# Optimization experiments

Hardware: AMD Instinct MI355X
Metric: run time of the kernel (lower is better)

The kernel has to match this reference:

```python
import jax, jax.numpy as jnp
import numpy as np

B, H, W = 4, 256, 256
DIM = 180
NH = 6
WH, WW = 16, 16          # window size
BH, BW = 8, 8            # base window size
CH = DIM // (2 * NH)     # per-head dim = 15
SCALE = float(CH)        # note: divide by head_dim (not sqrt), as in source
RH, RW = WH // BH, WW // BW
R = RH * RW              # spatial reduction ratio = 4
L = WH * WW              # 256 tokens per window
BL = BH * BW             # 64 base tokens
POS_DIM = (DIM // 4) // 4  # 11


def _rel_index(Hs, Ws):
    coords = np.stack(np.meshgrid(np.arange(Hs), np.arange(Ws), indexing='ij')).reshape(2, -1)
    rel = (coords[:, :, None] - coords[:, None, :]).transpose(1, 2, 0)
    rel[..., 0] += Hs - 1
    rel[..., 1] += Ws - 1
    rel[..., 0] *= 2 * Ws - 1
    return rel.sum(-1)  # (L, L) int

RPI = _rel_index(WH, WW)


def _ln(x, g, b):
    mu = x.mean(-1, keepdims=True)
    var = ((x - mu) ** 2).mean(-1, keepdims=True)
    return (x - mu) / jnp.sqrt(var + 1e-5) * g + b


def _conv(x, w, b):  # x: NHWC, w: HWIO
    y = jax.lax.conv_general_dilated(x, w, (1, 1), 'SAME',
                                     dimension_numbers=('NHWC', 'HWIO', 'NHWC'))
    return y + b


def setup_inputs():
    key = jax.random.key(0)
    ks = jax.random.split(key, 12)
    def wgt(k, shape, s=0.05):
        return jax.random.normal(k, shape, jnp.float32) * s
    C5 = DIM // 5
    d = {}
    d['x'] = jax.random.normal(ks[0], (B, H, W, DIM), jnp.float32)
    d['dfe_c1_w'] = wgt(ks[1], (1, 1, DIM, C5)); d['dfe_c1_b'] = jnp.zeros((C5,), jnp.float32)
    d['dfe_c2_w'] = wgt(ks[2], (3, 3, C5, C5));  d['dfe_c2_b'] = jnp.zeros((C5,), jnp.float32)
    d['dfe_c3_w'] = wgt(ks[3], (1, 1, C5, DIM)); d['dfe_c3_b'] = jnp.zeros((DIM,), jnp.float32)
    d['dfe_lin_w'] = wgt(ks[4], (1, 1, DIM, DIM)); d['dfe_lin_b'] = jnp.zeros((DIM,), jnp.float32)
    d['sl_w'] = wgt(ks[5], (1, R), 0.5); d['sl_b'] = jnp.zeros((1,), jnp.float32)
    d['pos_proj_w'] = wgt(ks[6], (POS_DIM, 2), 0.1); d['pos_proj_b'] = jnp.zeros((POS_DIM,), jnp.float32)
    for i, kk in zip((1, 2), (ks[7], ks[8])):
        d['pos%d_ln_g' % i] = jnp.ones((POS_DIM,), jnp.float32)
        d['pos%d_ln_b' % i] = jnp.zeros((POS_DIM,), jnp.float32)
        d['pos%d_w' % i] = wgt(kk, (POS_DIM, POS_DIM), 0.1)
        d['pos%d_b' % i] = jnp.zeros((POS_DIM,), jnp.float32)
    d['pos3_ln_g'] = jnp.ones((POS_DIM,), jnp.float32)
    d['pos3_ln_b'] = jnp.zeros((POS_DIM,), jnp.float32)
    d['pos3_w'] = wgt(ks[9], (NH, POS_DIM), 0.1)
    d['pos3_b'] = jnp.zeros((NH,), jnp.float32)
    d['proj_w'] = wgt(ks[10], (DIM, DIM))
    d['proj_b'] = jnp.zeros((DIM,), jnp.float32)
    return d


def reference(x, dfe_c1_w, dfe_c1_b, dfe_c2_w, dfe_c2_b, dfe_c3_w, dfe_c3_b,
              dfe_lin_w, dfe_lin_b, sl_w, sl_b, pos_proj_w, pos_proj_b,
              pos1_ln_g, pos1_ln_b, pos1_w, pos1_b,
              pos2_ln_g, pos2_ln_b, pos2_w, pos2_b,
              pos3_ln_g, pos3_ln_b, pos3_w, pos3_b,
              proj_w, proj_b):
    Bb, Hh, Ww_, C = x.shape
    # ---- DFE: qv = conv_path(x) * linear_path(x) ----
    t = jax.nn.leaky_relu(_conv(x, dfe_c1_w, dfe_c1_b), 0.2)
    t = jax.nn.leaky_relu(_conv(t, dfe_c2_w, dfe_c2_b), 0.2)
    t = _conv(t, dfe_c3_w, dfe_c3_b)
    qv = t * _conv(x, dfe_lin_w, dfe_lin_b)  # (B,H,W,C)
    # ---- window partition ----
    qv = qv.reshape(Bb, Hh // WH, WH, Ww_ // WW, WW, C).transpose(0, 1, 3, 2, 4, 5)
    qv = qv.reshape(-1, L, C)                       # (B_, L, C)
    B_ = qv.shape[0]
    qv = qv.reshape(B_, L, 2, NH, CH)
    q = qv[:, :, 0].transpose(0, 2, 1, 3)           # (B_, NH, L, CH)
    v = qv[:, :, 1].transpose(0, 2, 1, 3)           # (B_, NH, L, CH)
    # ---- spatial linear projection of v to base window ----
    vp = v.reshape(B_, NH, BH, RH, BW, RW, CH).transpose(0, 1, 2, 4, 6, 3, 5)
    vp = vp.reshape(B_, NH, BL, CH, R)
    vp = jnp.einsum('bnlcr,r->bnlc', vp, sl_w[0]) + sl_b[0]  # (B_, NH, BL, CH)
    # ---- spatial self-correlation ----
    corr = jnp.einsum('bnlc,bnmc->bnlm', q, vp) / SCALE       # (B_, NH, L, BL)
    # dynamic relative position bias (non-residual MLP)
    ph = jnp.arange(1 - WH, WH)
    pw = jnp.arange(1 - WW, WW)
    biases = jnp.stack(jnp.meshgrid(ph, pw, indexing='ij')).reshape(2, -1).T.astype(x.dtype)
    p = biases @ pos_proj_w.T + pos_proj_b
    p = jax.nn.relu(_ln(p, pos1_ln_g, pos1_ln_b)) @ pos1_w.T + pos1_b
    p = jax.nn.relu(_ln(p, pos2_ln_g, pos2_ln_b)) @ pos2_w.T + pos2_b
    pos = jax.nn.relu(_ln(p, pos3_ln_g, pos3_ln_b)) @ pos3_w.T + pos3_b  # ((2WH-1)(2WW-1), NH)
    rpb = pos[RPI.reshape(-1)].reshape(L, L, NH).transpose(2, 0, 1)      # (NH, L, L)
    rpb = rpb.reshape(NH, L, BH, RH, BW, RW).transpose(0, 1, 2, 4, 3, 5)
    rpb = rpb.reshape(NH, L, BL, R).mean(-1)                             # (NH, L, BL)
    corr = corr + rpb[None]
    x_sp = jnp.einsum('bnlm,bnmc->bnlc', corr, vp)
    x_sp = x_sp.transpose(0, 2, 1, 3).reshape(B_, L, C // 2)
    # ---- channel self-correlation (single-head) ----
    qc = q.transpose(0, 2, 1, 3).reshape(B_, L, C // 2)
    vc = v.transpose(0, 2, 1, 3).reshape(B_, L, C // 2)
    cmap = jnp.einsum('blc,bld->bcd', qc, vc) / float(L)                 # (B_, C/2, C/2)
    x_ch = jnp.einsum('bcd,bld->blc', cmap, vc)                          # (B_, L, C/2)
    # ---- window reverse + fuse ----
    def rev(a):
        c = a.shape[-1]
        a = a.reshape(Bb, Hh // WH, Ww_ // WW, WH, WW, c).transpose(0, 1, 3, 2, 4, 5)
        return a.reshape(Bb, Hh, Ww_, c)
    x_sp = rev(x_sp.reshape(B_, WH, WW, C // 2))
    x_ch = rev(x_ch.reshape(B_, WH, WW, C // 2))
    out = jnp.concatenate([x_sp, x_ch], -1) @ proj_w.T + proj_b          # (B,H,W,C)
    return out
```

## Files before the change

kernel.cpp:

```cpp
#include <hip/hip_runtime.h>

#define LEAKY(v) ((v) > 0.f ? (v) : 0.2f * (v))

__device__ __forceinline__ void ln_relu11(float* p, const float* __restrict__ g,
                                          const float* __restrict__ b) {
  float mu = 0.f;
#pragma unroll
  for (int j = 0; j < 11; ++j) mu += p[j];
  mu *= (1.f / 11.f);
  float var = 0.f;
#pragma unroll
  for (int j = 0; j < 11; ++j) { float d = p[j] - mu; var += d * d; }
  var *= (1.f / 11.f);
  float inv = 1.f / sqrtf(var + 1e-5f);
#pragma unroll
  for (int j = 0; j < 11; ++j) {
    float v = (p[j] - mu) * inv * g[j] + b[j];
    p[j] = v > 0.f ? v : 0.f;
  }
}

__global__ void pos_mlp_kernel(
    const float* __restrict__ w0, const float* __restrict__ b0,
    const float* __restrict__ g1, const float* __restrict__ be1,
    const float* __restrict__ w1, const float* __restrict__ b1,
    const float* __restrict__ g2, const float* __restrict__ be2,
    const float* __restrict__ w2, const float* __restrict__ b2,
    const float* __restrict__ g3, const float* __restrict__ be3,
    const float* __restrict__ w3, const float* __restrict__ b3,
    float* __restrict__ pos_out) {
  int r = blockIdx.x * 256 + threadIdx.x;
  if (r >= 961) return;
  float bh = (float)(r / 31 - 15);
  float bw = (float)(r % 31 - 15);
  float p[11], q[11];
#pragma unroll
  for (int j = 0; j < 11; ++j) p[j] = bh * w0[2 * j] + bw * w0[2 * j + 1] + b0[j];
  ln_relu11(p, g1, be1);
#pragma unroll
  for (int j = 0; j < 11; ++j) {
    float s = b1[j];
#pragma unroll
    for (int k = 0; k < 11; ++k) s += p[k] * w1[j * 11 + k];
    q[j] = s;
  }
  ln_relu11(q, g2, be2);
#pragma unroll
  for (int j = 0; j < 11; ++j) {
    float s = b2[j];
#pragma unroll
    for (int k = 0; k < 11; ++k) s += q[k] * w2[j * 11 + k];
    p[j] = s;
  }
  ln_relu11(p, g3, be3);
#pragma unroll
  for (int n = 0; n < 6; ++n) {
    float s = b3[n];
#pragma unroll
    for (int k = 0; k < 11; ++k) s += p[k] * w3[n * 11 + k];
    pos_out[r * 6 + n] = s;
  }
}

__global__ void rpb_kernel(const float* __restrict__ pos, float* __restrict__ rpb) {
  int o = blockIdx.x * 256 + threadIdx.x;
  int n = o >> 14;
  int l = (o >> 6) & 255;
  int m = o & 63;
  int i1 = l >> 4, j1 = l & 15;
  int bi = m >> 3, bj = m & 7;
  float s = 0.f;
#pragma unroll
  for (int rh = 0; rh < 2; ++rh)
#pragma unroll
    for (int rw = 0; rw < 2; ++rw) {
      int i2 = bi * 2 + rh, j2 = bj * 2 + rw;
      int idx = (i1 - i2 + 15) * 31 + (j1 - j2 + 15);
      s += pos[idx * 6 + n];
    }
  rpb[o] = s * 0.25f;
}

__global__ void pt_kernel(const float* __restrict__ pjw, float* __restrict__ pt) {
  int i = blockIdx.x * 256 + threadIdx.x;
  if (i >= 180 * 180) return;
  int c = i / 180, k = i % 180;
  pt[c * 180 + k] = pjw[k * 180 + c];
}

__global__ __launch_bounds__(256) void dfe1_kernel(const float* __restrict__ x,
                                                   const float* __restrict__ w1,
                                                   const float* __restrict__ b1,
                                                   float* __restrict__ t1) {
  __shared__ float xt[256][36];
  int t = threadIdx.x;
  int p0 = blockIdx.x * 256;
  float acc[36];
#pragma unroll
  for (int j = 0; j < 36; ++j) acc[j] = 0.f;
  for (int kc = 0; kc < 5; ++kc) {
    __syncthreads();
    for (int idx = t; idx < 256 * 36; idx += 256) {
      int px = idx / 36, ci = idx % 36;
      xt[px][ci] = x[(p0 + px) * 180 + kc * 36 + ci];
    }
    __syncthreads();
    for (int ci = 0; ci < 36; ++ci) {
      float v = xt[t][ci];
      const float* wr = &w1[(kc * 36 + ci) * 36];
#pragma unroll
      for (int j = 0; j < 36; ++j) acc[j] += v * wr[j];
    }
  }
  float* o = &t1[(p0 + t) * 36];
#pragma unroll
  for (int j = 0; j < 36; ++j) {
    float v = acc[j] + b1[j];
    o[j] = LEAKY(v);
  }
}

__global__ __launch_bounds__(256) void dfe2_kernel(const float* __restrict__ t1,
                                                   const float* __restrict__ w2,
                                                   const float* __restrict__ b2,
                                                   float* __restrict__ t2) {
  __shared__ float halo[18][18][36];
  int t = threadIdx.x;
  int blk = blockIdx.x;
  int img = blk >> 8;
  int rem = blk & 255;
  int ty0 = (rem >> 4) << 4;
  int tx0 = (rem & 15) << 4;
  for (int idx = t; idx < 18 * 18 * 36; idx += 256) {
    int ci = idx % 36;
    int xx = (idx / 36) % 18;
    int yy = idx / (36 * 18);
    int gy = ty0 + yy - 1;
    int gx = tx0 + xx - 1;
    float v = 0.f;
    if (gy >= 0 && gy < 256 && gx >= 0 && gx < 256)
      v = t1[((img * 256 + gy) * 256 + gx) * 36 + ci];
    halo[yy][xx][ci] = v;
  }
  __syncthreads();
  int ly = t >> 4, lx = t & 15;
  float acc[36];
#pragma unroll
  for (int j = 0; j < 36; ++j) acc[j] = 0.f;
#pragma unroll
  for (int kh = 0; kh < 3; ++kh)
#pragma unroll
    for (int kw = 0; kw < 3; ++kw) {
      for (int ci = 0; ci < 36; ++ci) {
        float v = halo[ly + kh][lx + kw][ci];
        const float* wr = &w2[((kh * 3 + kw) * 36 + ci) * 36];
#pragma unroll
        for (int j = 0; j < 36; ++j) acc[j] += v * wr[j];
      }
    }
  float* o = &t2[((img * 256 + ty0 + ly) * 256 + tx0 + lx) * 36];
#pragma unroll
  for (int j = 0; j < 36; ++j) {
    float v = acc[j] + b2[j];
    o[j] = LEAKY(v);
  }
}

__global__ __launch_bounds__(256, 4) void dfe3_kernel(const float* __restrict__ x,
                                                      const float* __restrict__ t2,
                                                      const float* __restrict__ w3,
                                                      const float* __restrict__ b3,
                                                      const float* __restrict__ wl,
                                                      const float* __restrict__ bl,
                                                      float* __restrict__ qv) {
  __shared__ __align__(16) float As[36 * 68];
  __shared__ __align__(16) float Bs[36 * 180 + 16];
  int t = threadIdx.x;
  int tx = t & 15;
  int ty = t >> 4;
  int p0 = blockIdx.x * 64;

  int pa0 = t / 9,          ca0 = t - pa0 * 9;
  int pa1 = (t + 256) / 9,  ca1 = (t + 256) - pa1 * 9;
  int pa2 = (t + 512) / 9,  ca2 = (t + 512) - pa2 * 9;
  const float4* xf4  = (const float4*)x;
  const float4* t2f4 = (const float4*)t2;
  const float4* wlf4 = (const float4*)wl;
  const float4* w3f4 = (const float4*)w3;
  float4* Bs4 = (float4*)Bs;

  float4 aR0, aR1, aR2;
  float4 bR0, bR1, bR2, bR3, bR4, bR5, bR6;
  aR2 = make_float4(0.f, 0.f, 0.f, 0.f);
  bR6 = make_float4(0.f, 0.f, 0.f, 0.f);

  auto stage_write = [&]() {
    As[(ca0 * 4 + 0) * 68 + pa0] = aR0.x;
    As[(ca0 * 4 + 1) * 68 + pa0] = aR0.y;
    As[(ca0 * 4 + 2) * 68 + pa0] = aR0.z;
    As[(ca0 * 4 + 3) * 68 + pa0] = aR0.w;
    As[(ca1 * 4 + 0) * 68 + pa1] = aR1.x;
    As[(ca1 * 4 + 1) * 68 + pa1] = aR1.y;
    As[(ca1 * 4 + 2) * 68 + pa1] = aR1.z;
    As[(ca1 * 4 + 3) * 68 + pa1] = aR1.w;
    if (t < 64) {
      As[(ca2 * 4 + 0) * 68 + pa2] = aR2.x;
      As[(ca2 * 4 + 1) * 68 + pa2] = aR2.y;
      As[(ca2 * 4 + 2) * 68 + pa2] = aR2.z;
      As[(ca2 * 4 + 3) * 68 + pa2] = aR2.w;
    }
    Bs4[t] = bR0;
    Bs4[t + 256] = bR1;
    Bs4[t + 512] = bR2;
    Bs4[t + 768] = bR3;
    Bs4[t + 1024] = bR4;
    Bs4[t + 1280] = bR5;
    if (t < 84) Bs4[t + 1536] = bR6;
  };

  auto compute36 = [&](float acc[4][12]) {
    for (int ci = 0; ci < 36; ++ci) {
      float4 a = *(const float4*)&As[ci * 68 + ty * 4];
      const float* bp = &Bs[ci * 180 + tx * 12];
      float4 b0 = *(const float4*)bp;
      float4 b1 = *(const float4*)(bp + 4);
      float4 b2 = *(const float4*)(bp + 8);
      float av[4] = {a.x, a.y, a.z, a.w};
      float bv[12] = {b0.x, b0.y, b0.z, b0.w, b1.x, b1.y, b1.z, b1.w,
                      b2.x, b2.y, b2.z, b2.w};
#pragma unroll
      for (int r = 0; r < 4; ++r)
#pragma unroll
        for (int j = 0; j < 12; ++j) acc[r][j] += av[r] * bv[j];
    }
  };

  aR0 = xf4[(size_t)(p0 + pa0) * 45 + ca0];
  aR1 = xf4[(size_t)(p0 + pa1) * 45 + ca1];
  if (t < 64) aR2 = xf4[(size_t)(p0 + pa2) * 45 + ca2];
  bR0 = wlf4[t];
  bR1 = wlf4[t + 256];
  bR2 = wlf4[t + 512];
  bR3 = wlf4[t + 768];
  bR4 = wlf4[t + 1024];
  bR5 = wlf4[t + 1280];
  if (t < 84) bR6 = wlf4[t + 1536];

  float accL[4][12], accC[4][12];
#pragma unroll
  for (int r = 0; r < 4; ++r)
#pragma unroll
    for (int j = 0; j < 12; ++j) accL[r][j] = 0.f;

#pragma unroll 1
  for (int p = 0; p < 5; ++p) {
    stage_write();
    __syncthreads();
    if (p < 4) {
      int kb = (p + 1) * 9;
      aR0 = xf4[(size_t)(p0 + pa0) * 45 + kb + ca0];
      aR1 = xf4[(size_t)(p0 + pa1) * 45 + kb + ca1];
      if (t < 64) aR2 = xf4[(size_t)(p0 + pa2) * 45 + kb + ca2];
      int kw = (p + 1) * 1620;
      bR0 = wlf4[kw + t];
      bR1 = wlf4[kw + t + 256];
      bR2 = wlf4[kw + t + 512];
      bR3 = wlf4[kw + t + 768];
      bR4 = wlf4[kw + t + 1024];
      bR5 = wlf4[kw + t + 1280];
      if (t < 84) bR6 = wlf4[kw + t + 1536];
    } else {
      aR0 = t2f4[(size_t)(p0 + pa0) * 9 + ca0];
      aR1 = t2f4[(size_t)(p0 + pa1) * 9 + ca1];
      if (t < 64) aR2 = t2f4[(size_t)(p0 + pa2) * 9 + ca2];
      bR0 = w3f4[t];
      bR1 = w3f4[t + 256];
      bR2 = w3f4[t + 512];
      bR3 = w3f4[t + 768];
      bR4 = w3f4[t + 1024];
      bR5 = w3f4[t + 1280];
      if (t < 84) bR6 = w3f4[t + 1536];
    }
    compute36(accL);
    __syncthreads();
  }

#pragma unroll
  for (int r = 0; r < 4; ++r)
#pragma unroll
    for (int j = 0; j < 12; ++j) accC[r][j] = 0.f;
  stage_write();
  __syncthreads();
  compute36(accC);

  if (tx < 15) {
#pragma unroll
    for (int r = 0; r < 4; ++r) {
      int base = (p0 + ty * 4 + r) * 180 + tx * 12;
#pragma unroll
      for (int j = 0; j < 12; ++j) {
        int co = tx * 12 + j;
        float cp = accC[r][j] + b3[co];
        float lp = accL[r][j] + bl[co];
        qv[base + j] = cp * lp;
      }
    }
  }
}

__global__ __launch_bounds__(256, 4) void att_sp_kernel(
    const float* __restrict__ qv, const float* __restrict__ slw,
    const float* __restrict__ slb, const float* __restrict__ rpb,
    const float* __restrict__ pt, const float* __restrict__ pb,
    float* __restrict__ out) {
  __shared__ __align__(16) float vp[6][64][16];
  __shared__ float xsp[128][91];
  int t = threadIdx.x;
  int wb = blockIdx.x;
  int b = wb >> 8, wi = (wb >> 4) & 15, wj = wb & 15;
  int wbase = (b * 256 + wi * 16) * 256 + wj * 16;
  float wsl0 = slw[0], wsl1 = slw[1], wsl2 = slw[2], wsl3 = slw[3];
  float bsl = slb[0];

  for (int idx = t; idx < 6 * 64 * 16; idx += 256) {
    int n = idx >> 10;
    int m = (idx >> 4) & 63;
    int ch = idx & 15;
    float s = 0.f;
    if (ch < 15) {
      int bi = m >> 3, bj = m & 7;
      int pa00 = (wbase + (bi * 2) * 256 + bj * 2) * 180 + 90 + n * 15 + ch;
      s = qv[pa00] * wsl0;
      s += qv[pa00 + 180] * wsl1;
      s += qv[pa00 + 256 * 180] * wsl2;
      s += qv[pa00 + 257 * 180] * wsl3;
      s += bsl;
    }
    vp[n][m][ch] = s;
  }
  __syncthreads();

  int lt = t & 127;
  int hg = t >> 7;
  const float inv15 = 1.f / 15.f;

#pragma unroll 1
  for (int half = 0; half < 2; ++half) {
    int l = half * 128 + lt;
    int pa = (wbase + (l >> 4) * 256 + (l & 15)) * 180;
#pragma unroll 1
    for (int nn = 0; nn < 3; ++nn) {
      int n = hg * 3 + nn;
      float qh[15];
#pragma unroll
      for (int c = 0; c < 15; ++c) qh[c] = qv[pa + n * 15 + c];
      float xs[15];
#pragma unroll
      for (int c = 0; c < 15; ++c) xs[c] = 0.f;
      const float* rp = &rpb[(n * 256 + l) * 64];
#pragma unroll 4
      for (int m4 = 0; m4 < 16; ++m4) {
        float4 rpv = *(const float4*)(rp + m4 * 4);
        float rparr[4] = {rpv.x, rpv.y, rpv.z, rpv.w};
#pragma unroll
        for (int mm = 0; mm < 4; ++mm) {
          const float4* vr = (const float4*)(&vp[n][m4 * 4 + mm][0]);
          float4 v0 = vr[0], v1 = vr[1], v2 = vr[2], v3 = vr[3];
          float s = qh[0] * v0.x + qh[1] * v0.y + qh[2] * v0.z + qh[3] * v0.w +
                    qh[4] * v1.x + qh[5] * v1.y + qh[6] * v1.z + qh[7] * v1.w +
                    qh[8] * v2.x + qh[9] * v2.y + qh[10] * v2.z + qh[11] * v2.w +
                    qh[12] * v3.x + qh[13] * v3.y + qh[14] * v3.z;
          s = s * inv15 + rparr[mm];
          xs[0] += s * v0.x; xs[1] += s * v0.y; xs[2] += s * v0.z; xs[3] += s * v0.w;
          xs[4] += s * v1.x; xs[5] += s * v1.y; xs[6] += s * v1.z; xs[7] += s * v1.w;
          xs[8] += s * v2.x; xs[9] += s * v2.y; xs[10] += s * v2.z; xs[11] += s * v2.w;
          xs[12] += s * v3.x; xs[13] += s * v3.y; xs[14] += s * v3.z;
        }
      }
#pragma unroll
      for (int c = 0; c < 15; ++c) xsp[lt][n * 15 + c] = xs[c];
    }
    __syncthreads();
    {
      int lane = t & 63;
      int w4 = __builtin_amdgcn_readfirstlane(t >> 6);
      int k0 = w4 * 45;
      const float* ptb = pt + k0;
#pragma unroll 1
      for (int tok2 = 0; tok2 < 2; ++tok2) {
        int tt = tok2 * 64 + lane;
        int l2 = half * 128 + tt;
        int pa2 = (wbase + (l2 >> 4) * 256 + (l2 & 15)) * 180 + k0;
        float pacc[45];
#pragma unroll
        for (int j = 0; j < 45; ++j) pacc[j] = pb[k0 + j];
#pragma unroll 2
        for (int c = 0; c < 90; ++c) {
          float xv = xsp[tt][c];
          const float* pr = ptb + c * 180;
#pragma unroll
          for (int j = 0; j < 45; ++j) pacc[j] += xv * pr[j];
        }
        float* op = out + pa2;
#pragma unroll
        for (int j = 0; j < 45; ++j) op[j] = pacc[j];
      }
    }
    __syncthreads();
  }
}

__global__ __launch_bounds__(256, 2) void cmapM_kernel(const float* __restrict__ qv,
                                                       const float* __restrict__ p2t,
                                                       float* __restrict__ M) {
  __shared__ float cmt[90][91];
  __shared__ float bufA[32][97];
  __shared__ float vtt[32][97];
  int t = threadIdx.x;
  int wb = blockIdx.x;
  int b = wb >> 8, wi = (wb >> 4) & 15, wj = wb & 15;
  int wbase = (b * 256 + wi * 16) * 256 + wj * 16;

  int tx = t & 15, ty = t >> 4;
  float acc[6][6];
#pragma unroll
  for (int i = 0; i < 6; ++i)
#pragma unroll
    for (int j = 0; j < 6; ++j) acc[i][j] = 0.f;

#pragma unroll 1
  for (int ck = 0; ck < 8; ++ck) {
    __syncthreads();
    for (int idx = t; idx < 32 * 97; idx += 256) {
      int l = idx / 97, c = idx % 97;
      int gl = ck * 32 + l;
      int pa = (wbase + (gl >> 4) * 256 + (gl & 15)) * 180;
      bufA[l][c] = (c < 90) ? qv[pa + c] : 0.f;
      vtt[l][c] = (c < 90) ? qv[pa + 90 + c] : 0.f;
    }
    __syncthreads();
    for (int lk = 0; lk < 32; ++lk) {
      float aa[6], bb[6];
#pragma unroll
      for (int i = 0; i < 6; ++i) aa[i] = bufA[lk][tx * 6 + i];
#pragma unroll
      for (int j = 0; j < 6; ++j) bb[j] = vtt[lk][ty * 6 + j];
#pragma unroll
      for (int i = 0; i < 6; ++i)
#pragma unroll
        for (int j = 0; j < 6; ++j) acc[i][j] += aa[i] * bb[j];
    }
  }
  __syncthreads();
  if (tx < 15 && ty < 15) {
#pragma unroll
    for (int i = 0; i < 6; ++i)
#pragma unroll
      for (int j = 0; j < 6; ++j) cmt[tx * 6 + i][ty * 6 + j] = acc[i][j] * (1.f / 256.f);
  }
  __syncthreads();

  int lane = t & 63;
  int kq = __builtin_amdgcn_readfirstlane(t >> 6);
  int k0 = kq * 45;
  int d0 = lane;
  int d1 = lane + 64;
  int d1c = (d1 < 90) ? d1 : 0;
  float m0[45], m1[45];
#pragma unroll
  for (int j = 0; j < 45; ++j) { m0[j] = 0.f; m1[j] = 0.f; }
#pragma unroll 1
  for (int c = 0; c < 90; ++c) {
    const float* pr = p2t + c * 180 + k0;
    float v0 = cmt[c][d0];
    float v1 = cmt[c][d1c];
#pragma unroll
    for (int j = 0; j < 45; ++j) {
      float p = pr[j];
      m0[j] += p * v0;
      m1[j] += p * v1;
    }
  }
  float* M0 = M + (size_t)wb * 16200 + d0 * 180 + k0;
#pragma unroll
  for (int j = 0; j < 45; ++j) M0[j] = m0[j];
  if (d1 < 90) {
    float* M1 = M + (size_t)wb * 16200 + d1 * 180 + k0;
#pragma unroll
    for (int j = 0; j < 45; ++j) M1[j] = m1[j];
  }
}

__global__ __launch_bounds__(256, 4) void chupd_kernel(const float* __restrict__ qv,
                                                       const float* __restrict__ M,
                                                       float* __restrict__ out) {
  __shared__ float vt[64][91];
  int bid = blockIdx.x;
  int wb = bid >> 2, grp = bid & 3;
  int b = wb >> 8, wi = (wb >> 4) & 15, wj = wb & 15;
  int wbase = (b * 256 + wi * 16) * 256 + wj * 16;
  int t = threadIdx.x;

  for (int idx = t; idx < 64 * 90; idx += 256) {
    int l = idx / 90, d = idx - l * 90;
    int gl = grp * 64 + l;
    int pa = (wbase + (gl >> 4) * 256 + (gl & 15)) * 180;
    vt[l][d] = qv[pa + 90 + d];
  }
  __syncthreads();

  int l = t & 63;
  int kq = __builtin_amdgcn_readfirstlane(t >> 6);
  int k0 = kq * 45;
  const float* Mw = M + (size_t)wb * 16200;
  float pacc[45];
#pragma unroll
  for (int j = 0; j < 45; ++j) pacc[j] = 0.f;
#pragma unroll 2
  for (int d = 0; d < 90; ++d) {
    const float* mr = Mw + d * 180 + k0;
    float vl = vt[l][d];
#pragma unroll
    for (int j = 0; j < 45; ++j) pacc[j] += mr[j] * vl;
  }
  int gl = grp * 64 + l;
  int pa = (wbase + (gl >> 4) * 256 + (gl & 15)) * 180 + k0;
#pragma unroll
  for (int j = 0; j < 45; ++j) out[pa + j] += pacc[j];
}

extern "C" void kernel_launch(void* const* d_in, const int* in_sizes, int n_in,
                              void* d_out, int out_size, void* d_ws, size_t ws_size,
                              hipStream_t stream) {
  (void)in_sizes; (void)n_in; (void)out_size; (void)ws_size;
  const float* x   = (const float*)d_in[0];
  const float* w1  = (const float*)d_in[1];
  const float* b1  = (const float*)d_in[2];
  const float* w2  = (const float*)d_in[3];
  const float* b2  = (const float*)d_in[4];
  const float* w3  = (const float*)d_in[5];
  const float* b3  = (const float*)d_in[6];
  const float* wl  = (const float*)d_in[7];
  const float* bl  = (const float*)d_in[8];
  const float* slw = (const float*)d_in[9];
  const float* slb = (const float*)d_in[10];
  const float* pw0 = (const float*)d_in[11];
  const float* pb0 = (const float*)d_in[12];
  const float* g1  = (const float*)d_in[13];
  const float* be1 = (const float*)d_in[14];
  const float* mw1 = (const float*)d_in[15];
  const float* mb1 = (const float*)d_in[16];
  const float* g2  = (const float*)d_in[17];
  const float* be2 = (const float*)d_in[18];
  const float* mw2 = (const float*)d_in[19];
  const float* mb2 = (const float*)d_in[20];
  const float* g3  = (const float*)d_in[21];
  const float* be3 = (const float*)d_in[22];
  const float* mw3 = (const float*)d_in[23];
  const float* mb3 = (const float*)d_in[24];
  const float* pjw = (const float*)d_in[25];
  const float* pjb = (const float*)d_in[26];
  float* out = (float*)d_out;
  float* ws  = (float*)d_ws;

  float* qv  = ws;
  float* t1  = ws + 47185920;
  float* t2  = t1 + 9437184;
  float* pos = t2 + 9437184;
  float* rpb = pos + 5768;
  float* M   = t1;
  float* pt  = t1 + 18874368 - 32768;

  pos_mlp_kernel<<<4, 256, 0, stream>>>(pw0, pb0, g1, be1, mw1, mb1,
                                        g2, be2, mw2, mb2, g3, be3, mw3, mb3, pos);
  rpb_kernel<<<384, 256, 0, stream>>>(pos, rpb);
  dfe1_kernel<<<1024, 256, 0, stream>>>(x, w1, b1, t1);
  dfe2_kernel<<<1024, 256, 0, stream>>>(t1, w2, b2, t2);
  dfe3_kernel<<<4096, 256, 0, stream>>>(x, t2, w3, b3, wl, bl, qv);
  pt_kernel<<<127, 256, 0, stream>>>(pjw, pt);
  att_sp_kernel<<<1024, 256, 0, stream>>>(qv, slw, slb, rpb, pt, pjb, out);
  cmapM_kernel<<<1024, 256, 0, stream>>>(qv, pt + 90 * 180, M);
  chupd_kernel<<<4096, 256, 0, stream>>>(qv, M, out);
}
```

Baseline: 1.375 ms.

## Enlarge dfe3 register tile to 8x12 and pair tokens per thread in attention

The dfe3 GEMM now gives each block 128 pixels and each thread an 8x12 register tile, halving the grid. To keep register pressure bounded, the linear-branch result is written to qv and re-read for the final multiply instead of holding two accumulator sets. att_sp now has each thread handle two adjacent tokens across three heads, so every shared-memory V load is reused twice. Both kernels drop to 2 blocks per CU in launch bounds, trading occupancy for more reuse per thread and risking register spills plus the extra global round trip in dfe3.

```diff
diff --git a/kernel.cpp b/kernel.cpp
--- a/kernel.cpp
+++ b/kernel.cpp
@@ -166,89 +166,110 @@
   }
 }
 
-__global__ __launch_bounds__(256, 4) void dfe3_kernel(const float* __restrict__ x,
+__global__ __launch_bounds__(256, 2) void dfe3_kernel(const float* __restrict__ x,
                                                       const float* __restrict__ t2,
                                                       const float* __restrict__ w3,
                                                       const float* __restrict__ b3,
                                                       const float* __restrict__ wl,
                                                       const float* __restrict__ bl,
                                                       float* __restrict__ qv) {
-  __shared__ __align__(16) float As[36 * 68];
+  __shared__ __align__(16) float As[36 * 132];
   __shared__ __align__(16) float Bs[36 * 180 + 16];
   int t = threadIdx.x;
   int tx = t & 15;
   int ty = t >> 4;
-  int p0 = blockIdx.x * 64;
-
-  int pa0 = t / 9,          ca0 = t - pa0 * 9;
-  int pa1 = (t + 256) / 9,  ca1 = (t + 256) - pa1 * 9;
-  int pa2 = (t + 512) / 9,  ca2 = (t + 512) - pa2 * 9;
+  int p0 = blockIdx.x * 128;
+
+  int pA0 = t / 9,           cA0 = t - pA0 * 9;
+  int pA1 = (t + 256) / 9,   cA1 = (t + 256) - pA1 * 9;
+  int pA2 = (t + 512) / 9,   cA2 = (t + 512) - pA2 * 9;
+  int pA3 = (t + 768) / 9,   cA3 = (t + 768) - pA3 * 9;
+  int pA4 = (t + 1024) / 9,  cA4 = (t + 1024) - pA4 * 9;
   const float4* xf4  = (const float4*)x;
   const float4* t2f4 = (const float4*)t2;
   const float4* wlf4 = (const float4*)wl;
   const float4* w3f4 = (const float4*)w3;
   float4* Bs4 = (float4*)Bs;
 
-  float4 aR0, aR1, aR2;
-  float4 bR0, bR1, bR2, bR3, bR4, bR5, bR6;
-  aR2 = make_float4(0.f, 0.f, 0.f, 0.f);
-  bR6 = make_float4(0.f, 0.f, 0.f, 0.f);
-
+  float4 a0, a1, a2, a3, a4;
+  float4 bF0, bF1, bF2, bF3, bF4, bF5, bF6;
+  a4 = make_float4(0.f, 0.f, 0.f, 0.f);
+  bF6 = make_float4(0.f, 0.f, 0.f, 0.f);
+
+  auto scatterA = [&](int pa, int ca, float4 v) {
+    As[(ca * 4 + 0) * 132 + pa] = v.x;
+    As[(ca * 4 + 1) * 132 + pa] = v.y;
+    As[(ca * 4 + 2) * 132 + pa] = v.z;
+    As[(ca * 4 + 3) * 132 + pa] = v.w;
+  };
   auto stage_write = [&]() {
-    As[(ca0 * 4 + 0) * 68 + pa0] = aR0.x;
-    As[(ca0 * 4 + 1) * 68 + pa0] = aR0.y;
-    As[(ca0 * 4 + 2) * 68 + pa0] = aR0.z;
-    As[(ca0 * 4 + 3) * 68 + pa0] = aR0.w;
-    As[(ca1 * 4 + 0) * 68 + pa1] = aR1.x;
-    As[(ca1 * 4 + 1) * 68 + pa1] = aR1.y;
-    As[(ca1 * 4 + 2) * 68 + pa1] = aR1.z;
-    As[(ca1 * 4 + 3) * 68 + pa1] = aR1.w;
-    if (t < 64) {
-      As[(ca2 * 4 + 0) * 68 + pa2] = aR2.x;
-      As[(ca2 * 4 + 1) * 68 + pa2] = aR2.y;
-      As[(ca2 * 4 + 2) * 68 + pa2] = aR2.z;
-      As[(ca2 * 4 + 3) * 68 + pa2] = aR2.w;
-    }
-    Bs4[t] = bR0;
-    Bs4[t + 256] = bR1;
-    Bs4[t + 512] = bR2;
-    Bs4[t + 768] = bR3;
-    Bs4[t + 1024] = bR4;
-    Bs4[t + 1280] = bR5;
-    if (t < 84) Bs4[t + 1536] = bR6;
+    scatterA(pA0, cA0, a0);
+    scatterA(pA1, cA1, a1);
+    scatterA(pA2, cA2, a2);
+    scatterA(pA3, cA3, a3);
+    if (t < 128) scatterA(pA4, cA4, a4);
+    Bs4[t] = bF0;
+    Bs4[t + 256] = bF1;
+    Bs4[t + 512] = bF2;
+    Bs4[t + 768] = bF3;
+    Bs4[t + 1024] = bF4;
+    Bs4[t + 1280] = bF5;
+    if (t < 84) Bs4[t + 1536] = bF6;
   };
 
-  auto compute36 = [&](float acc[4][12]) {
+  auto issue_lin = [&](int kc) {
+    int kb = kc * 9;
+    a0 = xf4[(size_t)(p0 + pA0) * 45 + kb + cA0];
+    a1 = xf4[(size_t)(p0 + pA1) * 45 + kb + cA1];
+    a2 = xf4[(size_t)(p0 + pA2) * 45 + kb + cA2];
+    a3 = xf4[(size_t)(p0 + pA3) * 45 + kb + cA3];
+    if (t < 128) a4 = xf4[(size_t)(p0 + pA4) * 45 + kb + cA4];
+    int kw = kc * 1620;
+    bF0 = wlf4[kw + t];
+    bF1 = wlf4[kw + t + 256];
+    bF2 = wlf4[kw + t + 512];
+    bF3 = wlf4[kw + t + 768];
+    bF4 = wlf4[kw + t + 1024];
+    bF5 = wlf4[kw + t + 1280];
+    if (t < 84) bF6 = wlf4[kw + t + 1536];
+  };
+  auto issue_conv = [&]() {
+    a0 = t2f4[(size_t)(p0 + pA0) * 9 + cA0];
+    a1 = t2f4[(size_t)(p0 + pA1) * 9 + cA1];
+    a2 = t2f4[(size_t)(p0 + pA2) * 9 + cA2];
+    a3 = t2f4[(size_t)(p0 + pA3) * 9 + cA3];
+    if (t < 128) a4 = t2f4[(size_t)(p0 + pA4) * 9 + cA4];
+    bF0 = w3f4[t];
+    bF1 = w3f4[t + 256];
+    bF2 = w3f4[t + 512];
+    bF3 = w3f4[t + 768];
+    bF4 = w3f4[t + 1024];
+    bF5 = w3f4[t + 1280];
+    if (t < 84) bF6 = w3f4[t + 1536];
+  };
+
+  auto compute36 = [&](float acc[8][12]) {
     for (int ci = 0; ci < 36; ++ci) {
-      float4 a = *(const float4*)&As[ci * 68 + ty * 4];
+      const float4* ap = (const float4*)&As[ci * 132 + ty * 8];
+      float4 A0 = ap[0], A1 = ap[1];
       const float* bp = &Bs[ci * 180 + tx * 12];
-      float4 b0 = *(const float4*)bp;
-      float4 b1 = *(const float4*)(bp + 4);
-      float4 b2 = *(const float4*)(bp + 8);
-      float av[4] = {a.x, a.y, a.z, a.w};
-      float bv[12] = {b0.x, b0.y, b0.z, b0.w, b1.x, b1.y, b1.z, b1.w,
-                      b2.x, b2.y, b2.z, b2.w};
-#pragma unroll
-      for (int r = 0; r < 4; ++r)
+      float4 B0 = *(const float4*)bp;
+      float4 B1 = *(const float4*)(bp + 4);
+      float4 B2 = *(const float4*)(bp + 8);
+      float av[8] = {A0.x, A0.y, A0.z, A0.w, A1.x, A1.y, A1.z, A1.w};
+      float bv[12] = {B0.x, B0.y, B0.z, B0.w, B1.x, B1.y, B1.z, B1.w,
+                      B2.x, B2.y, B2.z, B2.w};
+#pragma unroll
+      for (int r = 0; r < 8; ++r)
 #pragma unroll
         for (int j = 0; j < 12; ++j) acc[r][j] += av[r] * bv[j];
     }
   };
 
-  aR0 = xf4[(size_t)(p0 + pa0) * 45 + ca0];
-  aR1 = xf4[(size_t)(p0 + pa1) * 45 + ca1];
-  if (t < 64) aR2 = xf4[(size_t)(p0 + pa2) * 45 + ca2];
-  bR0 = wlf4[t];
-  bR1 = wlf4[t + 256];
-  bR2 = wlf4[t + 512];
-  bR3 = wlf4[t + 768];
-  bR4 = wlf4[t + 1024];
-  bR5 = wlf4[t + 1280];
-  if (t < 84) bR6 = wlf4[t + 1536];
-
-  float accL[4][12], accC[4][12];
-#pragma unroll
-  for (int r = 0; r < 4; ++r)
+  issue_lin(0);
+  float accL[8][12];
+#pragma unroll
+  for (int r = 0; r < 8; ++r)
 #pragma unroll
     for (int j = 0; j < 12; ++j) accL[r][j] = 0.f;
 
@@ -256,37 +277,23 @@
   for (int p = 0; p < 5; ++p) {
     stage_write();
     __syncthreads();
-    if (p < 4) {
-      int kb = (p + 1) * 9;
-      aR0 = xf4[(size_t)(p0 + pa0) * 45 + kb + ca0];
-      aR1 = xf4[(size_t)(p0 + pa1) * 45 + kb + ca1];
-      if (t < 64) aR2 = xf4[(size_t)(p0 + pa2) * 45 + kb + ca2];
-      int kw = (p + 1) * 1620;
-      bR0 = wlf4[kw + t];
-      bR1 = wlf4[kw + t + 256];
-      bR2 = wlf4[kw + t + 512];
-      bR3 = wlf4[kw + t + 768];
-      bR4 = wlf4[kw + t + 1024];
-      bR5 = wlf4[kw + t + 1280];
-      if (t < 84) bR6 = wlf4[kw + t + 1536];
-    } else {
-      aR0 = t2f4[(size_t)(p0 + pa0) * 9 + ca0];
-      aR1 = t2f4[(size_t)(p0 + pa1) * 9 + ca1];
-      if (t < 64) aR2 = t2f4[(size_t)(p0 + pa2) * 9 + ca2];
-      bR0 = w3f4[t];
-      bR1 = w3f4[t + 256];
-      bR2 = w3f4[t + 512];
-      bR3 = w3f4[t + 768];
-      bR4 = w3f4[t + 1024];
-      bR5 = w3f4[t + 1280];
-      if (t < 84) bR6 = w3f4[t + 1536];
-    }
+    if (p < 4) issue_lin(p + 1); else issue_conv();
     compute36(accL);
     __syncthreads();
   }
 
-#pragma unroll
-  for (int r = 0; r < 4; ++r)
+  if (tx < 15) {
+#pragma unroll
+    for (int r = 0; r < 8; ++r) {
+      int base = (p0 + ty * 8 + r) * 180 + tx * 12;
+#pragma unroll
+      for (int j = 0; j < 12; ++j) qv[base + j] = accL[r][j] + bl[tx * 12 + j];
+    }
+  }
+
+  float accC[8][12];
+#pragma unroll
+  for (int r = 0; r < 8; ++r)
 #pragma unroll
     for (int j = 0; j < 12; ++j) accC[r][j] = 0.f;
   stage_write();
@@ -295,20 +302,18 @@
 
   if (tx < 15) {
 #pragma unroll
-    for (int r = 0; r < 4; ++r) {
-      int base = (p0 + ty * 4 + r) * 180 + tx * 12;
+    for (int r = 0; r < 8; ++r) {
+      int base = (p0 + ty * 8 + r) * 180 + tx * 12;
 #pragma unroll
       for (int j = 0; j < 12; ++j) {
-        int co = tx * 12 + j;
-        float cp = accC[r][j] + b3[co];
-        float lp = accL[r][j] + bl[co];
-        qv[base + j] = cp * lp;
+        float lp = qv[base + j];
+        qv[base + j] = (accC[r][j] + b3[tx * 12 + j]) * lp;
       }
     }
   }
 }
 
-__global__ __launch_bounds__(256, 4) void att_sp_kernel(
+__global__ __launch_bounds__(256, 2) void att_sp_kernel(
     const float* __restrict__ qv, const float* __restrict__ slw,
     const float* __restrict__ slb, const float* __restrict__ rpb,
     const float* __restrict__ pt, const float* __restrict__ pb,
@@ -340,45 +345,77 @@
   }
   __syncthreads();
 
-  int lt = t & 127;
-  int hg = t >> 7;
   const float inv15 = 1.f / 15.f;
+  int h0 = t >> 7;
+  int rem = t & 127;
+  int half = rem >> 6;
+  int pr = rem & 63;
+  int l0 = half * 128 + pr * 2;
+  int l1 = l0 + 1;
+  int pa0 = (wbase + (l0 >> 4) * 256 + (l0 & 15)) * 180;
+  int pa1 = (wbase + (l1 >> 4) * 256 + (l1 & 15)) * 180;
+
+  auto attn_unit = [&](int n, float (&xs0)[15], float (&xs1)[15]) {
+    float qh0[15], qh1[15];
+#pragma unroll
+    for (int c = 0; c < 15; ++c) {
+      qh0[c] = qv[pa0 + n * 15 + c];
+      qh1[c] = qv[pa1 + n * 15 + c];
+    }
+#pragma unroll
+    for (int c = 0; c < 15; ++c) { xs0[c] = 0.f; xs1[c] = 0.f; }
+    const float* rpA = &rpb[(n * 256 + l0) * 64];
+    const float* rpB = &rpb[(n * 256 + l1) * 64];
+#pragma unroll 2
+    for (int m4 = 0; m4 < 16; ++m4) {
+      float4 ra = *(const float4*)(rpA + m4 * 4);
+      float4 rb = *(const float4*)(rpB + m4 * 4);
+      float raa[4] = {ra.x, ra.y, ra.z, ra.w};
+      float rba[4] = {rb.x, rb.y, rb.z, rb.w};
+#pragma unroll
+      for (int mm = 0; mm < 4; ++mm) {
+        const float4* vr = (const float4*)(&vp[n][m4 * 4 + mm][0]);
+        float4 v0 = vr[0], v1 = vr[1], v2 = vr[2], v3 = vr[3];
+        float s0 = qh0[0] * v0.x + qh0[1] * v0.y + qh0[2] * v0.z + qh0[3] * v0.w +
+                   qh0[4] * v1.x + qh0[5] * v1.y + qh0[6] * v1.z + qh0[7] * v1.w +
+                   qh0[8] * v2.x + qh0[9] * v2.y + qh0[10] * v2.z + qh0[11] * v2.w +
+                   qh0[12] * v3.x + qh0[13] * v3.y + qh0[14] * v3.z;
+        float s1 = qh1[0] * v0.x + qh1[1] * v0.y + qh1[2] * v0.z + qh1[3] * v0.w +
+                   qh1[4] * v1.x + qh1[5] * v1.y + qh1[6] * v1.z + qh1[7] * v1.w +
+                   qh1[8] * v2.x + qh1[9] * v2.y + qh1[10] * v2.z + qh1[11] * v2.w +
+                   qh1[12] * v3.x + qh1[13] * v3.y + qh1[14] * v3.z;
+        s0 = s0 * inv15 + raa[mm];
+        s1 = s1 * inv15 + rba[mm];
+        xs0[0] += s0 * v0.x; xs0[1] += s0 * v0.y; xs0[2] += s0 * v0.z; xs0[3] += s0 * v0.w;
+        xs0[4] += s0 * v1.x; xs0[5] += s0 * v1.y; xs0[6] += s0 * v1.z; xs0[7] += s0 * v1.w;
+        xs0[8] += s0 * v2.x; xs0[9] += s0 * v2.y; xs0[10] += s0 * v2.z; xs0[11] += s0 * v2.w;
+        xs0[12] += s0 * v3.x; xs0[13] += s0 * v3.y; xs0[14] += s0 * v3.z;
+        xs1[0] += s1 * v0.x; xs1[1] += s1 * v0.y; xs1[2] += s1 * v0.z; xs1[3] += s1 * v0.w;
+        xs1[4] += s1 * v1.x; xs1[5] += s1 * v1.y; xs1[6] += s1 * v1.z; xs1[7] += s1 * v1.w;
+        xs1[8] += s1 * v2.x; xs1[9] += s1 * v2.y; xs1[10] += s1 * v2.z; xs1[11] += s1 * v2.w;
+        xs1[12] += s1 * v3.x; xs1[13] += s1 * v3.y; xs1[14] += s1 * v3.z;
+      }
+    }
+  };
+
+  float xsA0[15], xsA1[15], xsB0[15], xsB1[15], xsC0[15], xsC1[15];
+  attn_unit(h0, xsA0, xsA1);
+  attn_unit(h0 + 2, xsB0, xsB1);
+  attn_unit(h0 + 4, xsC0, xsC1);
 
 #pragma unroll 1
-  for (int half = 0; half < 2; ++half) {
-    int l = half * 128 + lt;
-    int pa = (wbase + (l >> 4) * 256 + (l & 15)) * 180;
-#pragma unroll 1
-    for (int nn = 0; nn < 3; ++nn) {
-      int n = hg * 3 + nn;
-      float qh[15];
-#pragma unroll
-      for (int c = 0; c < 15; ++c) qh[c] = qv[pa + n * 15 + c];
-      float xs[15];
-#pragma unroll
-      for (int c = 0; c < 15; ++c) xs[c] = 0.f;
-      const float* rp = &rpb[(n * 256 + l) * 64];
-#pragma unroll 4
-      for (int m4 = 0; m4 < 16; ++m4) {
-        float4 rpv = *(const float4*)(rp + m4 * 4);
-        float rparr[4] = {rpv.x, rpv.y, rpv.z, rpv.w};
-#pragma unroll
-        for (int mm = 0; mm < 4; ++mm) {
-          const float4* vr = (const float4*)(&vp[n][m4 * 4 + mm][0]);
-          float4 v0 = vr[0], v1 = vr[1], v2 = vr[2], v3 = vr[3];
-          float s = qh[0] * v0.x + qh[1] * v0.y + qh[2] * v0.z + qh[3] * v0.w +
-                    qh[4] * v1.x + qh[5] * v1.y + qh[6] * v1.z + qh[7] * v1.w +
-                    qh[8] * v2.x + qh[9] * v2.y + qh[10] * v2.z + qh[11] * v2.w +
-                    qh[12] * v3.x + qh[13] * v3.y + qh[14] * v3.z;
-          s = s * inv15 + rparr[mm];
-          xs[0] += s * v0.x; xs[1] += s * v0.y; xs[2] += s * v0.z; xs[3] += s * v0.w;
-          xs[4] += s * v1.x; xs[5] += s * v1.y; xs[6] += s * v1.z; xs[7] += s * v1.w;
-          xs[8] += s * v2.x; xs[9] += s * v2.y; xs[10] += s * v2.z; xs[11] += s * v2.w;
-          xs[12] += s * v3.x; xs[13] += s * v3.y; xs[14] += s * v3.z;
-        }
+  for (int hs = 0; hs < 2; ++hs) {
+    if (half == hs) {
+      int r0 = pr * 2, r1 = r0 + 1;
+#pragma unroll
+      for (int c = 0; c < 15; ++c) {
+        xsp[r0][h0 * 15 + c] = xsA0[c];
+        xsp[r1][h0 * 15 + c] = xsA1[c];
+        xsp[r0][(h0 + 2) * 15 + c] = xsB0[c];
+        xsp[r1][(h0 + 2) * 15 + c] = xsB1[c];
+        xsp[r0][(h0 + 4) * 15 + c] = xsC0[c];
+        xsp[r1][(h0 + 4) * 15 + c] = xsC1[c];
       }
-#pragma unroll
-      for (int c = 0; c < 15; ++c) xsp[lt][n * 15 + c] = xs[c];
     }
     __syncthreads();
     {
@@ -389,7 +426,7 @@
 #pragma unroll 1
       for (int tok2 = 0; tok2 < 2; ++tok2) {
         int tt = tok2 * 64 + lane;
-        int l2 = half * 128 + tt;
+        int l2 = hs * 128 + tt;
         int pa2 = (wbase + (l2 >> 4) * 256 + (l2 & 15)) * 180 + k0;
         float pacc[45];
 #pragma unroll
@@ -397,9 +434,9 @@
 #pragma unroll 2
         for (int c = 0; c < 90; ++c) {
           float xv = xsp[tt][c];
-          const float* pr = ptb + c * 180;
-#pragma unroll
-          for (int j = 0; j < 45; ++j) pacc[j] += xv * pr[j];
+          const float* prw = ptb + c * 180;
+#pragma unroll
+          for (int j = 0; j < 45; ++j) pacc[j] += xv * prw[j];
         }
         float* op = out + pa2;
 #pragma unroll
@@ -576,7 +613,7 @@
   rpb_kernel<<<384, 256, 0, stream>>>(pos, rpb);
   dfe1_kernel<<<1024, 256, 0, stream>>>(x, w1, b1, t1);
   dfe2_kernel<<<1024, 256, 0, stream>>>(t1, w2, b2, t2);
-  dfe3_kernel<<<4096, 256, 0, stream>>>(x, t2, w3, b3, wl, bl, qv);
+  dfe3_kernel<<<2048, 256, 0, stream>>>(x, t2, w3, b3, wl, bl, qv);
   pt_kernel<<<127, 256, 0, stream>>>(pjw, pt);
   att_sp_kernel<<<1024, 256, 0, stream>>>(qv, slw, slb, rpb, pt, pjb, out);
   cmapM_kernel<<<1024, 256, 0, stream>>>(qv, pt + 90 * 180, M);
```

Measured after the change: 1.419 ms. 3.2% more time.
